# Kernel tuning notes

Hardware: AMD Instinct MI355X
Metric: run time of the kernel (lower is better)

The kernel has to match this reference:

```python
import jax, jax.numpy as jnp
import numpy as np

SUB, E_NO, I_NO = 20, 2000, 500
T_DATA, T_SYN, T_HIST = 20000, 200, 50
SB, HB = 3, 3


def setup_inputs() -> dict:
    key = jax.random.key(0)
    ks = jax.random.split(key, 14)
    S_e = (jax.random.uniform(ks[0], (T_DATA, E_NO)) < 0.02).astype(jnp.float32)
    S_i = (jax.random.uniform(ks[1], (T_DATA, I_NO)) < 0.02).astype(jnp.float32)
    C_den = (jax.random.uniform(ks[2], (SUB, SUB)) < 0.1).astype(jnp.float32)
    C_syn_e = (jax.random.uniform(ks[3], (SUB, E_NO)) < 0.05).astype(jnp.float32)
    C_syn_i = (jax.random.uniform(ks[4], (SUB, I_NO)) < 0.05).astype(jnp.float32)
    W_syn = 0.1 * jax.random.normal(ks[5], (SUB, SB, 2))
    Tau_syn = jnp.tile(jnp.arange(SB, dtype=jnp.float32)[:, None], (1, 2))
    Delta_syn = jax.random.uniform(ks[6], (SUB, 2))
    W_hist = 0.1 * jax.random.normal(ks[7], (SUB, HB))
    Tau_hist = jnp.arange(HB, dtype=jnp.float32)
    Delta_hist = jax.random.uniform(ks[8], (SUB,))
    W_sub = jax.random.uniform(ks[9], (SUB,))
    V_o = jax.random.normal(ks[10], (1,))
    Theta = jnp.zeros((SUB,), jnp.float32)
    return {"S_e": S_e, "S_i": S_i, "C_den": C_den, "C_syn_e": C_syn_e,
            "C_syn_i": C_syn_i, "W_syn": W_syn, "Tau_syn": Tau_syn,
            "Delta_syn": Delta_syn, "W_hist": W_hist, "Tau_hist": Tau_hist,
            "Delta_hist": Delta_hist, "W_sub": W_sub, "V_o": V_o, "Theta": Theta}


def _alpha_kernels(delta, tau_log, W, T):
    # delta: [sub], tau_log: [B], W: [sub, B] -> kernels [sub, T]
    t = jnp.maximum(jnp.arange(T, dtype=jnp.float32)[None, :] - delta[:, None], 0.0)  # [sub,T]
    tt = t[:, None, :] / jnp.exp(tau_log)[None, :, None]  # [sub,B,T]
    return jnp.einsum('sbt,sb->st', tt * jnp.exp(-tt), W)


def _causal_conv(x, kern):
    # x: [T, sub], kern: [sub, T_k]; out[t,s] = sum_k kern[s,k] * x[t-k,s]
    Tk = kern.shape[1]
    xp = jnp.pad(x.T[None], ((0, 0), (0, 0), (Tk - 1, 0)))  # [1, sub, T+Tk-1]
    out = jax.lax.conv_general_dilated(
        xp, jnp.flip(kern, 1)[:, None, :], (1,), 'VALID',
        feature_group_count=kern.shape[0])
    return out[0].T  # [T, sub]


def reference(S_e, S_i, C_den, C_syn_e, C_syn_i, W_syn, Tau_syn, Delta_syn,
              W_hist, Tau_hist, Delta_hist, W_sub, V_o, Theta):
    # --- synaptic drive (vectorized over subunits) ---
    ke = _alpha_kernels(jnp.exp(Delta_syn[:, 0]), Tau_syn[:, 0], W_syn[:, :, 0], T_SYN)
    ki = _alpha_kernels(jnp.exp(Delta_syn[:, 1]), Tau_syn[:, 1], W_syn[:, :, 1], T_SYN)
    in_e = S_e @ C_syn_e.T  # [T, sub]
    in_i = S_i @ C_syn_i.T
    syn_in = _causal_conv(in_e, ke) + _causal_conv(in_i, ki)  # [T, sub]

    # --- history kernel ---
    hist_kern = _alpha_kernels(Delta_hist, Tau_hist, W_hist, T_HIST)  # [sub, T_hist]
    K = jnp.flip(hist_kern, 1)  # K[s, j] multiplies buffer entry j (oldest first)

    # --- sequential recurrence via scan ---
    def step(buf, syn_t):
        # buf: [T_hist, sub] = Y_pad[t : t+T_hist]
        h = jnp.einsum('js,sj->s', buf, K)
        prop = (buf[-1] * W_sub) @ C_den.T
        y = jnp.tanh(syn_t + prop + Theta + h)
        buf = jnp.concatenate([buf[1:], y[None]], 0)
        return buf, y

    buf0 = jnp.zeros((T_HIST, SUB), syn_in.dtype)
    _, Y = jax.lax.scan(step, buf0, syn_in)  # Y: [T, sub]
    return Y[:, 0] * W_sub[0] + V_o[0]
```

## Files before the change

kernel.cpp:

```cpp
#include <hip/hip_runtime.h>
#include <hip/hip_bf16.h>
#include <stdint.h>
#include <type_traits>

#define SUBU 20
#define E_NO 2000
#define I_NO 500
#define T_DATA 20000
#define T_SYNK 200
#define HBAS 3
#define SBAS 3
#define TPAD 20096

#define OFF_SYN  0
#define OFF_INE  401920
#define OFF_INI  803840
#define OFF_KE   1205760
#define OFF_KI   1209760
#define OFF_IIR  1213760
#define OFF_MW   1214760
#define OFF_MIDX 1215000
#define OFF_PAR  1215240
#define OFF_FLAG 1215264
#define OFF_Y    OFF_INI
#define KSTORE   12

#define TKC 2.8853900817779268f

__device__ __forceinline__ float bf2f(unsigned short u){
  unsigned v = ((unsigned)u) << 16; float f; __builtin_memcpy(&f, &v, 4); return f;
}
__device__ __forceinline__ float ldany(const void* p, int i, int bf){
  return bf ? bf2f(((const unsigned short*)p)[i]) : ((const float*)p)[i];
}
__device__ __forceinline__ float ex2(float x){ return __builtin_amdgcn_exp2f(x); }
__device__ __forceinline__ float rcpa(float x){ return __builtin_amdgcn_rcpf(x); }

__global__ __launch_bounds__(512) void k_prep(
    const void* Se, const void* Cden, const void* Wsyn, const void* Tausyn,
    const void* Dsyn, const void* Whist, const void* Tauhist, const void* Dhist,
    const void* Wsub, const void* Vo, const void* Theta, float* ws){
  int* wsi = (int*)ws;
  const int tx = threadIdx.x;
  __shared__ int found, mx;
  if (tx == 0){ found = 0; mx = 0; }
  __syncthreads();
  {
    const unsigned* w = (const unsigned*)Se;
    int hit = 0;
    for (int i = tx; i < 8192; i += 512){
      unsigned x = w[i];
      if (x == 0x00003F80u || x == 0x3F803F80u) hit = 1;
    }
    if (hit) atomicOr(&found, 1);
  }
  __syncthreads();
  const int bf = found;
  if (tx == 0) wsi[OFF_FLAG] = bf;
  for (int idx = tx; idx < SUBU * T_SYNK; idx += 512){
    int s = idx / T_SYNK, t = idx % T_SYNK;
    for (int c = 0; c < 2; ++c){
      float delta = __expf(ldany(Dsyn, s*2 + c, bf));
      float acc = 0.f;
      for (int b = 0; b < SBAS; ++b){
        float tau = __expf(ldany(Tausyn, b*2 + c, bf));
        float w   = ldany(Wsyn, (s*SBAS + b)*2 + c, bf);
        float tt  = fmaxf((float)t - delta, 0.f) / tau;
        acc += w * tt * __expf(-tt);
      }
      ws[(c == 0 ? OFF_KE : OFF_KI) + s*T_SYNK + t] = acc;
    }
  }
  if (tx < SUBU * HBAS){
    int s = tx / HBAS, b = tx % HBAS;
    float tau = __expf(ldany(Tauhist, b, bf));
    float w   = TKC * ldany(Whist, s*HBAS + b, bf);
    float dl  = ldany(Dhist, s, bf);
    float rho = __expf(-1.f / tau);
    float e1  = __expf(-(1.f - dl) / tau);
    float g1  = ((1.f - dl) / tau) * e1;
    float kap = rho / tau;
    float* c = ws + OFF_IIR + s*16 + b*4;
    c[0] = rho;
    c[1] = w * kap;
    c[2] = w * g1;
    c[3] = e1;
    if (b == 2){
      float e49 = __expf(-(49.f - dl) / tau);
      float g49 = ((49.f - dl) / tau) * e49;
      ws[OFF_IIR + s*16 + 12] = w * (rho*g49 + kap*e49);
      ws[OFF_IIR + s*16 + 13] = rho * e49;
    }
  }
  if (tx < SUBU){
    int s = tx, cnt = 0;
    float rowsum = 0.f;
    for (int sp = 0; sp < SUBU; ++sp){
      float c = ldany(Cden, s*SUBU + sp, bf);
      if (c != 0.f && cnt < KSTORE){
        float m = c * ldany(Wsub, sp, bf);
        rowsum += m;
        ws[OFF_MW + s*KSTORE + cnt]  = -2.f * TKC * m;
        wsi[OFF_MIDX + s*KSTORE + cnt] = sp;
        ++cnt;
      }
    }
    for (int k = cnt; k < KSTORE; ++k){
      ws[OFF_MW + s*KSTORE + k] = 0.f; wsi[OFF_MIDX + s*KSTORE + k] = 0;
    }
    atomicMax(&mx, cnt);
    ws[OFF_PAR + s] = TKC * (ldany(Theta, s, bf) + rowsum);
  }
  __syncthreads();
  if (tx == 0){
    ws[OFF_PAR + SUBU]     = ldany(Wsub, 0, bf);
    ws[OFF_PAR + SUBU + 1] = ldany(Vo, 0, bf);
    wsi[OFF_PAR + 23] = (mx <= 3) ? 3 : (mx <= 4 ? 4 : (mx <= 6 ? 6 : 12));
  }
}

template<int BF>
__device__ __forceinline__ void gemm_impl(const void* S, const void* C, int W,
                                          float* dst, int t0, int lane){
  float acc[4][SUBU];
  #pragma unroll
  for (int r = 0; r < 4; ++r)
    #pragma unroll
    for (int s = 0; s < SUBU; ++s) acc[r][s] = 0.f;
  for (int e = lane; e < W; e += 64){
    float s0 = ldany(S, (t0+0)*W + e, BF);
    float s1 = ldany(S, (t0+1)*W + e, BF);
    float s2 = ldany(S, (t0+2)*W + e, BF);
    float s3 = ldany(S, (t0+3)*W + e, BF);
    #pragma unroll
    for (int s = 0; s < SUBU; ++s){
      float c = ldany(C, s*W + e, BF);
      acc[0][s] = fmaf(s0, c, acc[0][s]);
      acc[1][s] = fmaf(s1, c, acc[1][s]);
      acc[2][s] = fmaf(s2, c, acc[2][s]);
      acc[3][s] = fmaf(s3, c, acc[3][s]);
    }
  }
  #pragma unroll
  for (int r = 0; r < 4; ++r){
    #pragma unroll
    for (int s = 0; s < SUBU; ++s){
      float v = acc[r][s];
      #pragma unroll
      for (int m = 32; m >= 1; m >>= 1) v += __shfl_xor(v, m, 64);
      if (lane == 0) dst[s*TPAD + t0 + r] = v;
    }
  }
}

__global__ __launch_bounds__(256) void k_gemm(const void* S, const void* C, int W,
                                              float* dst, const int* flagp){
  const int wave = threadIdx.x >> 6, lane = threadIdx.x & 63;
  const int t0 = blockIdx.x * 16 + wave * 4;
  if (*flagp) gemm_impl<1>(S, C, W, dst, t0, lane);
  else        gemm_impl<0>(S, C, W, dst, t0, lane);
}

__global__ __launch_bounds__(256) void k_conv(float* ws){
  const int s  = blockIdx.y;
  const int t0 = blockIdx.x * 256;
  const float* ine = ws + OFF_INE + s*TPAD;
  const float* ini = ws + OFF_INI + s*TPAD;
  __shared__ float eL[455], iL[455], keL[T_SYNK], kiL[T_SYNK];
  for (int j = threadIdx.x; j < 455; j += 256){
    int t = t0 - 199 + j;
    bool ok = (t >= 0 && t < TPAD);
    eL[j] = ok ? ine[t] : 0.f;
    iL[j] = ok ? ini[t] : 0.f;
  }
  for (int j = threadIdx.x; j < T_SYNK; j += 256){
    keL[j] = ws[OFF_KE + s*T_SYNK + j];
    kiL[j] = ws[OFF_KI + s*T_SYNK + j];
  }
  __syncthreads();
  int t = t0 + threadIdx.x;
  if (t < TPAD){
    float a0 = 0.f, a1 = 0.f;
    #pragma unroll 4
    for (int k = 0; k < T_SYNK; ++k){
      a0 = fmaf(keL[k], eL[threadIdx.x + 199 - k], a0);
      a1 = fmaf(kiL[k], iL[threadIdx.x + 199 - k], a1);
    }
    ws[OFF_SYN + s*TPAD + t] = fmaf(TKC, a0 + a1, ws[OFF_PAR + s]);
  }
}

__device__ __forceinline__ float get4(const float4& a, const float4& b,
                                      const float4& c, const float4& d, int u){
  const float4& q = (u < 4) ? a : ((u < 8) ? b : ((u < 12) ? c : d));
  int r = u & 3;
  return (r == 0) ? q.x : ((r == 1) ? q.y : ((r == 2) ? q.z : q.w));
}
__device__ __forceinline__ void set4(float4& a, float4& b, float4& c, float4& d,
                                     int u, float v){
  float4& q = (u < 4) ? a : ((u < 8) ? b : ((u < 12) ? c : d));
  int r = u & 3;
  if (r == 0) q.x = v; else if (r == 1) q.y = v; else if (r == 2) q.z = v; else q.w = v;
}

template<int KM>
__global__ __launch_bounds__(64, 1) void k_scan(float* ws, float* yout){
  const int* wsi = (const int*)ws;
  if (wsi[OFF_PAR + 23] != KM) return;
  const int lane = threadIdx.x;
  const int s = lane < SUBU ? lane : SUBU - 1;
  float mwp[KM]; int mad[KM];
  #pragma unroll
  for (int k = 0; k < KM; ++k){
    mwp[k] = ws[OFF_MW + s*KSTORE + k];
    mad[k] = wsi[OFF_MIDX + s*KSTORE + k] * 4;
  }
  const float* cc = ws + OFF_IIR + s*16;
  const float rh0 = cc[0], kp0 = cc[1], ayc0 = cc[2], eyc0 = cc[3];
  const float rh1 = cc[4], kp1 = cc[5], ayc1 = cc[6], eyc1 = cc[7];
  const float rh2 = cc[8], kp2 = cc[9];
  const float cA = cc[12], cE = cc[13];
  const float ayr0 = -2.f*ayc0, eyr0 = -2.f*eyc0;
  const float ayr1 = -2.f*ayc1, eyr1 = -2.f*eyc1;
  const float ayr2 = -2.f*cc[10], eyr2 = -2.f*cc[11];
  const float cAr = 2.f*cA, cEr = 2.f*cE;
  const float c2A = cc[10] - cA;
  const float c2E = cc[11] - cE;
  const float wsub0 = ws[OFF_PAR + SUBU];
  const float vo    = ws[OFF_PAR + SUBU + 1];
  const float m2w = -2.f * wsub0, wvo = wsub0 + vo;
  const float* syncol = ws + OFF_SYN + s*TPAD;

  float rhv[82];
  #pragma unroll
  for (int j = 0; j < 82; ++j) rhv[j] = 0.5f;
  float A0=0.f,E0=0.f,A1=0.f,E1=0.f,A2=0.f,E2=0.f;
  float pb[KM];
  #pragma unroll
  for (int k = 0; k < KM; ++k) pb[k] = 0.5f;
  float4 u0 = *(const float4*)(syncol + 0);
  float4 u1 = *(const float4*)(syncol + 4);
  float4 u2 = *(const float4*)(syncol + 8);
  float4 u3 = *(const float4*)(syncol + 12);
  float4 n0, n1, n2, n3;
  float xpre = u0.x;

  auto block16 = [&](auto OFS_, int tbase, float4& b0, float4& b1, float4& b2,
                     float4& b3, float4& p0, float4& p1, float4& p2, float4& p3){
    constexpr int OFS = decltype(OFS_)::value;
    const float4* src = (const float4*)(syncol + tbase + 16);
    p0 = src[0]; p1 = src[1]; p2 = src[2]; p3 = src[3];
    float4 ob0, ob1, ob2, ob3;
    #pragma unroll
    for (int u = 0; u < 16; ++u){
      float acc0 = fmaf(mwp[0], pb[0], xpre);
      float acc1 = mwp[1] * pb[1];
      #pragma unroll
      for (int k = 2; k < KM; ++k){
        if (k & 1) acc1 = fmaf(mwp[k], pb[k], acc1);
        else       acc0 = fmaf(mwp[k], pb[k], acc0);
      }
      float X  = acc0 + acc1;
      float r  = rcpa(ex2(X) + 1.f);
      int rb = __float_as_int(r);
      #pragma unroll
      for (int k = 0; k < KM; ++k)
        pb[k] = __int_as_float(__builtin_amdgcn_ds_bpermute(mad[k], rb));
      float rp = rhv[OFS + u + 49];
      float ro = rhv[OFS + u];
      float A0n = fmaf(rh0, A0, fmaf(kp0, E0, fmaf(ayr0, rp, ayc0)));
      E0 = fmaf(rh0, E0, fmaf(eyr0, rp, eyc0)); A0 = A0n;
      float A1n = fmaf(rh1, A1, fmaf(kp1, E1, fmaf(ayr1, rp, ayc1)));
      E1 = fmaf(rh1, E1, fmaf(eyr1, rp, eyc1)); A1 = A1n;
      float A2n = fmaf(rh2, A2, fmaf(kp2, E2, fmaf(ayr2, rp, fmaf(cAr, ro, c2A))));
      E2 = fmaf(rh2, E2, fmaf(eyr2, rp, fmaf(cEr, ro, c2E))); A2 = A2n;
      float h = (A0 + A1) + A2;
      float cn = (u < 15) ? get4(b0, b1, b2, b3, u + 1) : p0.x;
      xpre = cn + h;
      rhv[OFS + u + 50] = r;
      set4(ob0, ob1, ob2, ob3, u, fmaf(r, m2w, wvo));
    }
    if (lane == 0 && tbase + 16 <= T_DATA){
      float4* q = (float4*)(yout + tbase);
      q[0] = ob0; q[1] = ob1; q[2] = ob2; q[3] = ob3;
    }
  };

  using IC0  = std::integral_constant<int,0>;
  using IC16 = std::integral_constant<int,16>;
  #pragma unroll 1
  for (int ib = 0; ib < 628; ++ib){
    block16(IC0{},  ib*32,      u0, u1, u2, u3, n0, n1, n2, n3);
    block16(IC16{}, ib*32 + 16, n0, n1, n2, n3, u0, u1, u2, u3);
    #pragma unroll
    for (int j = 0; j < 50; ++j) rhv[j] = rhv[j + 32];
  }
}

__global__ __launch_bounds__(256) void k_out(const float* ws, void* outp){
  const int* wsi = (const int*)ws;
  const int bf = wsi[OFF_FLAG];
  int i = blockIdx.x * 256 + threadIdx.x;
  if (i < T_DATA){
    float v = ws[OFF_Y + i];
    if (bf) ((__hip_bfloat16*)outp)[i] = __float2bfloat16(v);
    else    ((float*)outp)[i] = v;
  }
}

extern "C" void kernel_launch(void* const* d_in, const int* in_sizes, int n_in,
                              void* d_out, int out_size, void* d_ws, size_t ws_size,
                              hipStream_t stream){
  const void* S_e   = d_in[0];
  const void* S_i   = d_in[1];
  const void* C_den = d_in[2];
  const void* C_e   = d_in[3];
  const void* C_i   = d_in[4];
  const void* W_syn = d_in[5];
  const void* Tau_s = d_in[6];
  const void* D_syn = d_in[7];
  const void* W_hst = d_in[8];
  const void* Tau_h = d_in[9];
  const void* D_hst = d_in[10];
  const void* W_sub = d_in[11];
  const void* V_o   = d_in[12];
  const void* Theta = d_in[13];
  float* ws = (float*)d_ws;
  int* flagp = (int*)(ws + OFF_FLAG);

  k_prep<<<1, 512, 0, stream>>>(S_e, C_den, W_syn, Tau_s, D_syn, W_hst, Tau_h,
                                D_hst, W_sub, V_o, Theta, ws);
  k_gemm<<<1250, 256, 0, stream>>>(S_e, C_e, E_NO, ws + OFF_INE, flagp);
  k_gemm<<<1250, 256, 0, stream>>>(S_i, C_i, I_NO, ws + OFF_INI, flagp);
  dim3 cgrid(79, 20);
  k_conv<<<cgrid, 256, 0, stream>>>(ws);
  float* yout = ws + OFF_Y;
  k_scan<3><<<1, 64, 0, stream>>>(ws, yout);
  k_scan<4><<<1, 64, 0, stream>>>(ws, yout);
  k_scan<6><<<1, 64, 0, stream>>>(ws, yout);
  k_scan<12><<<1, 64, 0, stream>>>(ws, yout);
  k_out<<<79, 256, 0, stream>>>(ws, d_out);
}
```

Before: 2.125 ms.

## Replace register history shift with LDS ring buffer and add KM=5 scan variant

The 82-entry register history array, which was shifted by 32 every 32 steps, is replaced with a 64-entry per-lane ring buffer in shared memory. The loop is unrolled to four 16-step blocks so the ring offsets stay compile-time constants. The IIR history update is rewritten to work on y = 1-2r directly, dropping the precomputed constant offsets. A KM=5 specialisation is also added so inputs with a maximum dendritic fan-in of 5 no longer fall through to the 6-wide variant. This removes register pressure and the per-iteration 50 moves, but adds an LDS store and load to the serial critical path.

```diff
diff --git a/kernel.cpp b/kernel.cpp
--- a/kernel.cpp
+++ b/kernel.cpp
@@ -115,7 +115,8 @@
   if (tx == 0){
     ws[OFF_PAR + SUBU]     = ldany(Wsub, 0, bf);
     ws[OFF_PAR + SUBU + 1] = ldany(Vo, 0, bf);
-    wsi[OFF_PAR + 23] = (mx <= 3) ? 3 : (mx <= 4 ? 4 : (mx <= 6 ? 6 : 12));
+    wsi[OFF_PAR + 23] = (mx <= 3) ? 3 : (mx <= 4 ? 4 : (mx <= 5 ? 5 :
+                        (mx <= 6 ? 6 : 12)));
   }
 }
 
@@ -207,8 +208,16 @@
 __global__ __launch_bounds__(64, 1) void k_scan(float* ws, float* yout){
   const int* wsi = (const int*)ws;
   if (wsi[OFF_PAR + 23] != KM) return;
+  __shared__ float ring[64*68];
   const int lane = threadIdx.x;
   const int s = lane < SUBU ? lane : SUBU - 1;
+  float* rbase = &ring[lane*68];
+  {
+    float4 z = make_float4(0.f, 0.f, 0.f, 0.f);
+    float4* rq = (float4*)rbase;
+    #pragma unroll
+    for (int j = 0; j < 16; ++j) rq[j] = z;
+  }
   float mwp[KM]; int mad[KM];
   #pragma unroll
   for (int k = 0; k < KM; ++k){
@@ -216,28 +225,20 @@
     mad[k] = wsi[OFF_MIDX + s*KSTORE + k] * 4;
   }
   const float* cc = ws + OFF_IIR + s*16;
-  const float rh0 = cc[0], kp0 = cc[1], ayc0 = cc[2], eyc0 = cc[3];
-  const float rh1 = cc[4], kp1 = cc[5], ayc1 = cc[6], eyc1 = cc[7];
-  const float rh2 = cc[8], kp2 = cc[9];
-  const float cA = cc[12], cE = cc[13];
-  const float ayr0 = -2.f*ayc0, eyr0 = -2.f*eyc0;
-  const float ayr1 = -2.f*ayc1, eyr1 = -2.f*eyc1;
-  const float ayr2 = -2.f*cc[10], eyr2 = -2.f*cc[11];
-  const float cAr = 2.f*cA, cEr = 2.f*cE;
-  const float c2A = cc[10] - cA;
-  const float c2E = cc[11] - cE;
+  const float rh0 = cc[0],  kp0 = cc[1],  ay0 = cc[2],  ey0 = cc[3];
+  const float rh1 = cc[4],  kp1 = cc[5],  ay1 = cc[6],  ey1 = cc[7];
+  const float rh2 = cc[8],  kp2 = cc[9],  ay2 = cc[10], ey2 = cc[11];
+  const float cA  = cc[12], cE  = cc[13];
   const float wsub0 = ws[OFF_PAR + SUBU];
   const float vo    = ws[OFF_PAR + SUBU + 1];
-  const float m2w = -2.f * wsub0, wvo = wsub0 + vo;
   const float* syncol = ws + OFF_SYN + s*TPAD;
 
-  float rhv[82];
-  #pragma unroll
-  for (int j = 0; j < 82; ++j) rhv[j] = 0.5f;
   float A0=0.f,E0=0.f,A1=0.f,E1=0.f,A2=0.f,E2=0.f;
   float pb[KM];
   #pragma unroll
   for (int k = 0; k < KM; ++k) pb[k] = 0.5f;
+  float yprev = 0.f;
+  float roN   = 0.f;
   float4 u0 = *(const float4*)(syncol + 0);
   float4 u1 = *(const float4*)(syncol + 4);
   float4 u2 = *(const float4*)(syncol + 8);
@@ -245,9 +246,9 @@
   float4 n0, n1, n2, n3;
   float xpre = u0.x;
 
-  auto block16 = [&](auto OFS_, int tbase, float4& b0, float4& b1, float4& b2,
+  auto block16 = [&](auto PH_, int tbase, float4& b0, float4& b1, float4& b2,
                      float4& b3, float4& p0, float4& p1, float4& p2, float4& p3){
-    constexpr int OFS = decltype(OFS_)::value;
+    constexpr int PH = decltype(PH_)::value;
     const float4* src = (const float4*)(syncol + tbase + 16);
     p0 = src[0]; p1 = src[1]; p2 = src[2]; p3 = src[3];
     float4 ob0, ob1, ob2, ob3;
@@ -266,19 +267,21 @@
       #pragma unroll
       for (int k = 0; k < KM; ++k)
         pb[k] = __int_as_float(__builtin_amdgcn_ds_bpermute(mad[k], rb));
-      float rp = rhv[OFS + u + 49];
-      float ro = rhv[OFS + u];
-      float A0n = fmaf(rh0, A0, fmaf(kp0, E0, fmaf(ayr0, rp, ayc0)));
-      E0 = fmaf(rh0, E0, fmaf(eyr0, rp, eyc0)); A0 = A0n;
-      float A1n = fmaf(rh1, A1, fmaf(kp1, E1, fmaf(ayr1, rp, ayc1)));
-      E1 = fmaf(rh1, E1, fmaf(eyr1, rp, eyc1)); A1 = A1n;
-      float A2n = fmaf(rh2, A2, fmaf(kp2, E2, fmaf(ayr2, rp, fmaf(cAr, ro, c2A))));
-      E2 = fmaf(rh2, E2, fmaf(eyr2, rp, fmaf(cEr, ro, c2E))); A2 = A2n;
+      float y = fmaf(-2.f, r, 1.f);
+      float ro = roN;
+      float A0n = fmaf(rh0, A0, fmaf(kp0, E0, ay0 * yprev));
+      E0 = fmaf(rh0, E0, ey0 * yprev); A0 = A0n;
+      float A1n = fmaf(rh1, A1, fmaf(kp1, E1, ay1 * yprev));
+      E1 = fmaf(rh1, E1, ey1 * yprev); A1 = A1n;
+      float A2n = fmaf(rh2, A2, fmaf(kp2, E2, fmaf(-cA, ro, ay2 * yprev)));
+      E2 = fmaf(rh2, E2, fmaf(-cE, ro, ey2 * yprev)); A2 = A2n;
       float h = (A0 + A1) + A2;
       float cn = (u < 15) ? get4(b0, b1, b2, b3, u + 1) : p0.x;
       xpre = cn + h;
-      rhv[OFS + u + 50] = r;
-      set4(ob0, ob1, ob2, ob3, u, fmaf(r, m2w, wvo));
+      rbase[PH + u] = y;
+      roN = rbase[(PH + u + 15) & 63];
+      yprev = y;
+      set4(ob0, ob1, ob2, ob3, u, fmaf(y, wsub0, vo));
     }
     if (lane == 0 && tbase + 16 <= T_DATA){
       float4* q = (float4*)(yout + tbase);
@@ -286,14 +289,17 @@
     }
   };
 
-  using IC0  = std::integral_constant<int,0>;
-  using IC16 = std::integral_constant<int,16>;
+  using P0  = std::integral_constant<int,0>;
+  using P16 = std::integral_constant<int,16>;
+  using P32 = std::integral_constant<int,32>;
+  using P48 = std::integral_constant<int,48>;
   #pragma unroll 1
-  for (int ib = 0; ib < 628; ++ib){
-    block16(IC0{},  ib*32,      u0, u1, u2, u3, n0, n1, n2, n3);
-    block16(IC16{}, ib*32 + 16, n0, n1, n2, n3, u0, u1, u2, u3);
-    #pragma unroll
-    for (int j = 0; j < 50; ++j) rhv[j] = rhv[j + 32];
+  for (int ib2 = 0; ib2 < 314; ++ib2){
+    const int tb = ib2 * 64;
+    block16(P0{},  tb,      u0, u1, u2, u3, n0, n1, n2, n3);
+    block16(P16{}, tb + 16, n0, n1, n2, n3, u0, u1, u2, u3);
+    block16(P32{}, tb + 32, u0, u1, u2, u3, n0, n1, n2, n3);
+    block16(P48{}, tb + 48, n0, n1, n2, n3, u0, u1, u2, u3);
   }
 }
 
@@ -337,6 +343,7 @@
   float* yout = ws + OFF_Y;
   k_scan<3><<<1, 64, 0, stream>>>(ws, yout);
   k_scan<4><<<1, 64, 0, stream>>>(ws, yout);
+  k_scan<5><<<1, 64, 0, stream>>>(ws, yout);
   k_scan<6><<<1, 64, 0, stream>>>(ws, yout);
   k_scan<12><<<1, 64, 0, stream>>>(ws, yout);
   k_out<<<79, 256, 0, stream>>>(ws, d_out);
```

After: 1.995 ms. 1.07x faster.
